# Performance work log

Hardware: AMD Instinct MI355X
Metric: run time of the kernel (lower is better)

The kernel has to match this reference:

```python
import jax, jax.numpy as jnp
import numpy as np

B, C, N = 16, 128, 2048  # batch, channels (SA_Layer(128)), num points


def setup_inputs() -> dict:
    key = jax.random.key(0)
    ks = jax.random.split(key, 6)
    x = jax.random.normal(ks[0], (B, C, N), jnp.float32)
    wq = jax.random.normal(ks[1], (C // 4, C), jnp.float32) * 0.05  # shared q/k 1x1 conv, no bias
    wv = jax.random.normal(ks[2], (C, C), jnp.float32) * 0.05
    bv = jax.random.normal(ks[3], (C,), jnp.float32) * 0.05
    wt = jax.random.normal(ks[4], (C, C), jnp.float32) * 0.05
    bt = jax.random.normal(ks[5], (C,), jnp.float32) * 0.05
    gamma = jnp.ones((C,), jnp.float32)   # BatchNorm1d weight
    beta = jnp.zeros((C,), jnp.float32)   # BatchNorm1d bias
    bn_mean = jnp.zeros((C,), jnp.float32)  # running mean (eval mode)
    bn_var = jnp.ones((C,), jnp.float32)    # running var (eval mode)
    return dict(x=x, wq=wq, wv=wv, bv=bv, wt=wt, bt=bt,
                gamma=gamma, beta=beta, bn_mean=bn_mean, bn_var=bn_var)


def reference(x, wq, wv, bv, wt, bt, gamma, beta, bn_mean, bn_var):
    EPS = 1e-9
    BN_EPS = 1e-5
    # q_conv and k_conv share weights (tied in __init__)
    x_q = jnp.einsum('dc,bcn->bnd', wq, x)               # [B, N, C/4]
    x_k = jnp.einsum('dc,bcn->bdn', wq, x)               # [B, C/4, N]
    energy = jnp.einsum('bnd,bdm->bnm', x_q, x_k)        # [B, N, N]
    attn = jax.nn.softmax(energy, axis=-1)
    # offset-attention renormalization: divide by column sum
    attn = attn / (EPS + attn.sum(axis=1, keepdims=True))
    x_v = jnp.einsum('dc,bcn->bdn', wv, x) + bv[None, :, None]   # [B, C, N]
    x_r = jnp.einsum('bdn,bnm->bdm', x_v, attn)                  # [B, C, N]
    t = jnp.einsum('dc,bcn->bdn', wt, x - x_r) + bt[None, :, None]
    # BatchNorm1d (eval mode) + ReLU
    t = (t - bn_mean[None, :, None]) * jax.lax.rsqrt(bn_var + BN_EPS)[None, :, None]
    t = t * gamma[None, :, None] + beta[None, :, None]
    return x + jax.nn.relu(t)
```

## Files before the change

### kernel.cpp

```cpp
#include <hip/hip_runtime.h>
#include <hip/hip_bf16.h>
#include <math.h>

#define BB 16
#define CC 128
#define NN 2048
#define CQ 32

typedef __attribute__((ext_vector_type(8))) short bf16x8;
typedef __attribute__((ext_vector_type(4))) float f32x4;
typedef __attribute__((ext_vector_type(16))) float f32x16;

__device__ __forceinline__ ushort f2b(float f) {
    __hip_bfloat16 h = __float2bfloat16(f);
    return *reinterpret_cast<ushort*>(&h);
}
__device__ __forceinline__ float b2f(ushort u) {
    union { unsigned u; float f; } v; v.u = ((unsigned)u) << 16;
    return v.f;
}
__device__ __forceinline__ bf16x8 as_b8(uint4 u) {
    union { uint4 u; bf16x8 b; } v; v.u = u; return v.b;
}
__device__ __forceinline__ float fexp2(float x) {
    return __builtin_amdgcn_exp2f(x);
}

#define OFF_VB  524288
#define OFF_XRB 2621440
#define OFF_RSI 4718592

#define QSCALE 1.2011224087864498f

__global__ __launch_bounds__(256) void k_proj(const float* __restrict__ x,
        const float* __restrict__ wq, const float* __restrict__ wv,
        const float* __restrict__ bv, ushort* __restrict__ Qt, ushort* __restrict__ Vb) {
    __shared__ ushort Wl[160][136];
    __shared__ ushort Xs[64][136];
    int bid = (blockIdx.x & 7) * 64 + (blockIdx.x >> 3);
    int b  = bid >> 5;
    int n0 = (bid & 31) << 6;
    int tid = threadIdx.x;
    #pragma unroll
    for (int k = 0; k < 20; ++k) {
        int idx = k * 256 + tid;
        int r = idx >> 5, c4 = (idx & 31) << 2;
        const float* srcw = (r < 32) ? (wq + r * 128 + c4) : (wv + (r - 32) * 128 + c4);
        float4 w4 = *(const float4*)srcw;
        float s = (r < 32) ? QSCALE : 1.0f;
        *(ushort4*)&Wl[r][c4] = make_ushort4(f2b(w4.x * s), f2b(w4.y * s),
                                             f2b(w4.z * s), f2b(w4.w * s));
    }
    const float* xb = x + (size_t)b * CC * NN;
    for (int idx = tid; idx < 2048; idx += 256) {
        int c = idx >> 4, n4 = (idx & 15) << 2;
        float4 xv = *(const float4*)&xb[c * NN + n0 + n4];
        Xs[n4][c]     = f2b(xv.x);
        Xs[n4 + 1][c] = f2b(xv.y);
        Xs[n4 + 2][c] = f2b(xv.z);
        Xs[n4 + 3][c] = f2b(xv.w);
    }
    __syncthreads();
    int w = tid >> 6, l = tid & 63, lr = l & 15, lg = l >> 4;
    f32x4 zero = {0.f, 0.f, 0.f, 0.f};
    int nn = n0 + w * 16 + lr;
    for (int dt = 0; dt < 10; ++dt) {
        f32x4 acc = zero;
        #pragma unroll
        for (int k = 0; k < 4; ++k) {
            bf16x8 a  = *(const bf16x8*)&Wl[dt * 16 + lr][k * 32 + lg * 8];
            bf16x8 bx = *(const bf16x8*)&Xs[w * 16 + lr][k * 32 + lg * 8];
            acc = __builtin_amdgcn_mfma_f32_16x16x32_bf16(a, bx, acc, 0, 0, 0);
        }
        if (dt < 2) {
            ushort4 p = make_ushort4(f2b(acc[0]), f2b(acc[1]), f2b(acc[2]), f2b(acc[3]));
            *(ushort4*)&Qt[(size_t)(b * NN + nn) * CQ + dt * 16 + lg * 4] = p;
        } else {
            #pragma unroll
            for (int i = 0; i < 4; ++i) {
                int vd = (dt - 2) * 16 + lg * 4 + i;
                Vb[(size_t)(b * CC + vd) * NN + nn] = f2b(acc[i] + bv[vd]);
            }
        }
    }
}

__global__ __launch_bounds__(512) void k_rowstats(const ushort* __restrict__ Qt,
        float* __restrict__ RSI) {
    __shared__ ushort Qm[128][36];
    __shared__ float Sred[2][64];
    int bid = (blockIdx.x & 7) * 64 + (blockIdx.x >> 3);
    int b  = bid >> 5;
    int n0 = (bid & 31) << 6;
    int tid = threadIdx.x;
    int w = tid >> 6, l = tid & 63, lr = l & 15, lg = l >> 4;
    int wn = w & 3, wm = w >> 2;
    const ushort* Qtb = Qt + (size_t)b * NN * CQ;
    bf16x8 aq = *(const bf16x8*)&Qtb[(size_t)(n0 + wn * 16 + lr) * CQ + lg * 8];
    int sr = tid >> 2, sc = (tid & 3) * 8;
    uint4 q0 = *(const uint4*)&Qtb[(size_t)sr * CQ + sc];
    float S[4] = {0.f, 0.f, 0.f, 0.f};
    f32x4 zero = {0.f, 0.f, 0.f, 0.f};
    for (int t = 0; t < 16; ++t) {
        __syncthreads();
        *(uint4*)&Qm[sr][sc] = q0;
        __syncthreads();
        if (t < 15)
            q0 = *(const uint4*)&Qtb[(size_t)((t + 1) * 128 + sr) * CQ + sc];
        #pragma unroll
        for (int mi = 0; mi < 4; ++mi) {
            bf16x8 bq = *(const bf16x8*)&Qm[(wm * 4 + mi) * 16 + lr][lg * 8];
            f32x4 e = __builtin_amdgcn_mfma_f32_16x16x32_bf16(aq, bq, zero, 0, 0, 0);
            S[0] += fexp2(e[0]); S[1] += fexp2(e[1]);
            S[2] += fexp2(e[2]); S[3] += fexp2(e[3]);
        }
    }
    #pragma unroll
    for (int d = 1; d < 16; d <<= 1) {
        #pragma unroll
        for (int i = 0; i < 4; ++i) S[i] += __shfl_xor(S[i], d);
    }
    if (lr == 0) {
        #pragma unroll
        for (int i = 0; i < 4; ++i) Sred[wm][wn * 16 + lg * 4 + i] = S[i];
    }
    __syncthreads();
    if (tid < 64)
        RSI[b * NN + n0 + tid] = 1.f / (Sred[0][tid] + Sred[1][tid]);
}

__global__ __launch_bounds__(512, 4) void k_attn_pv(const ushort* __restrict__ Qt,
        const ushort* __restrict__ Vb, const float* __restrict__ RSI,
        ushort* __restrict__ XRb) {
    __shared__ ushort Vs[2][128][68];
    __shared__ ushort Ws[2][64][68];
    __shared__ float csred[4][64];
    __shared__ float csum[64];
    int bid = (blockIdx.x & 7) * 64 + (blockIdx.x >> 3);
    int b  = bid >> 5;
    int m0 = (bid & 31) << 6;
    int tid = threadIdx.x;
    int w = tid >> 6, l = tid & 63, lr = l & 15, lg = l >> 4;
    const ushort* Qtb = Qt + (size_t)b * NN * CQ;
    const ushort* Vbb = Vb + (size_t)b * CC * NN;
    const float*  RSb = RSI + (size_t)b * NN;
    f32x4 zero = {0.f, 0.f, 0.f, 0.f};
    bool producer = (w < 4);

    bf16x8 bm[4];
    float cs[4] = {0.f, 0.f, 0.f, 0.f};
    int sv = 0, shv = 0;
    const ushort* vsrc = nullptr;
    bf16x8 aq_nx; float4 rsi_nx;
    f32x16 pacc0, pacc1;
    int ar = l & 31, kh = l >> 5, dq = w - 4;

    if (producer) {
        #pragma unroll
        for (int mi = 0; mi < 4; ++mi)
            bm[mi] = *(const bf16x8*)&Qtb[(size_t)(m0 + mi * 16 + lr) * CQ + lg * 8];
        sv = tid >> 1; shv = (tid & 1) * 32;
        vsrc = Vbb + (size_t)sv * NN + shv;
        {
            uint4 v0 = *(const uint4*)(vsrc);
            uint4 v1 = *(const uint4*)(vsrc + 8);
            uint4 v2 = *(const uint4*)(vsrc + 16);
            uint4 v3 = *(const uint4*)(vsrc + 24);
            ushort* dst = &Vs[0][sv][shv];
            *(uint2*)(dst)      = make_uint2(v0.x, v0.y);
            *(uint2*)(dst + 4)  = make_uint2(v0.z, v0.w);
            *(uint2*)(dst + 8)  = make_uint2(v1.x, v1.y);
            *(uint2*)(dst + 12) = make_uint2(v1.z, v1.w);
            *(uint2*)(dst + 16) = make_uint2(v2.x, v2.y);
            *(uint2*)(dst + 20) = make_uint2(v2.z, v2.w);
            *(uint2*)(dst + 24) = make_uint2(v3.x, v3.y);
            *(uint2*)(dst + 28) = make_uint2(v3.z, v3.w);
        }
        {
            bf16x8 aq0 = *(const bf16x8*)&Qtb[(size_t)(w * 16 + lr) * CQ + lg * 8];
            float4 r4 = *(const float4*)&RSb[w * 16 + lg * 4];
            int nb = w * 16 + lg * 4;
            #pragma unroll
            for (int mi = 0; mi < 4; ++mi) {
                f32x4 e = __builtin_amdgcn_mfma_f32_16x16x32_bf16(aq0, bm[mi], zero, 0, 0, 0);
                float w0 = fexp2(e[0]) * r4.x;
                float w1 = fexp2(e[1]) * r4.y;
                float w2 = fexp2(e[2]) * r4.z;
                float w3 = fexp2(e[3]) * r4.w;
                cs[mi] += w0 + w1 + w2 + w3;
                *(ushort4*)&Ws[0][mi * 16 + lr][nb] =
                    make_ushort4(f2b(w0), f2b(w1), f2b(w2), f2b(w3));
            }
        }
        aq_nx  = *(const bf16x8*)&Qtb[(size_t)(64 + w * 16 + lr) * CQ + lg * 8];
        rsi_nx = *(const float4*)&RSb[64 + w * 16 + lg * 4];
    } else {
        #pragma unroll
        for (int r = 0; r < 16; ++r) { pacc0[r] = 0.f; pacc1[r] = 0.f; }
    }
    __syncthreads();
    for (int t = 0; t < 32; ++t) {
        int cur = t & 1;
        if (producer) {
            if (t < 31) {
                int ntn = (t + 1) * 64;
                uint4 v0 = *(const uint4*)(vsrc + ntn);
                uint4 v1 = *(const uint4*)(vsrc + ntn + 8);
                uint4 v2 = *(const uint4*)(vsrc + ntn + 16);
                uint4 v3 = *(const uint4*)(vsrc + ntn + 24);
                bf16x8 aq = aq_nx;
                float4 r4 = rsi_nx;
                if (t < 30) {
                    int nt2 = (t + 2) * 64;
                    aq_nx  = *(const bf16x8*)&Qtb[(size_t)(nt2 + w * 16 + lr) * CQ + lg * 8];
                    rsi_nx = *(const float4*)&RSb[nt2 + w * 16 + lg * 4];
                }
                int nb = w * 16 + lg * 4;
                #pragma unroll
                for (int mi = 0; mi < 4; ++mi) {
                    f32x4 e = __builtin_amdgcn_mfma_f32_16x16x32_bf16(aq, bm[mi], zero, 0, 0, 0);
                    float w0 = fexp2(e[0]) * r4.x;
                    float w1 = fexp2(e[1]) * r4.y;
                    float w2 = fexp2(e[2]) * r4.z;
                    float w3 = fexp2(e[3]) * r4.w;
                    cs[mi] += w0 + w1 + w2 + w3;
                    *(ushort4*)&Ws[cur ^ 1][mi * 16 + lr][nb] =
                        make_ushort4(f2b(w0), f2b(w1), f2b(w2), f2b(w3));
                }
                ushort* dst = &Vs[cur ^ 1][sv][shv];
                *(uint2*)(dst)      = make_uint2(v0.x, v0.y);
                *(uint2*)(dst + 4)  = make_uint2(v0.z, v0.w);
                *(uint2*)(dst + 8)  = make_uint2(v1.x, v1.y);
                *(uint2*)(dst + 12) = make_uint2(v1.z, v1.w);
                *(uint2*)(dst + 16) = make_uint2(v2.x, v2.y);
                *(uint2*)(dst + 20) = make_uint2(v2.z, v2.w);
                *(uint2*)(dst + 24) = make_uint2(v3.x, v3.y);
                *(uint2*)(dst + 28) = make_uint2(v3.z, v3.w);
            }
        } else {
            __builtin_amdgcn_s_setprio(1);
            #pragma unroll
            for (int kk = 0; kk < 4; ++kk) {
                const ushort* vp = &Vs[cur][dq * 32 + ar][kk * 16 + kh * 8];
                uint2 a0 = *(const uint2*)vp;
                uint2 a1 = *(const uint2*)(vp + 4);
                bf16x8 va = as_b8(make_uint4(a0.x, a0.y, a1.x, a1.y));
                const ushort* wp0 = &Ws[cur][ar][kk * 16 + kh * 8];
                uint2 b0 = *(const uint2*)wp0;
                uint2 b1 = *(const uint2*)(wp0 + 4);
                const ushort* wp1 = &Ws[cur][32 + ar][kk * 16 + kh * 8];
                uint2 c0 = *(const uint2*)wp1;
                uint2 c1 = *(const uint2*)(wp1 + 4);
                pacc0 = __builtin_amdgcn_mfma_f32_32x32x16_bf16(
                    va, as_b8(make_uint4(b0.x, b0.y, b1.x, b1.y)), pacc0, 0, 0, 0);
                pacc1 = __builtin_amdgcn_mfma_f32_32x32x16_bf16(
                    va, as_b8(make_uint4(c0.x, c0.y, c1.x, c1.y)), pacc1, 0, 0, 0);
            }
            __builtin_amdgcn_s_setprio(0);
        }
        __syncthreads();
    }
    if (producer) {
        #pragma unroll
        for (int mi = 0; mi < 4; ++mi) {
            cs[mi] += __shfl_xor(cs[mi], 16);
            cs[mi] += __shfl_xor(cs[mi], 32);
        }
        if (lg == 0) {
            #pragma unroll
            for (int mi = 0; mi < 4; ++mi) csred[w][mi * 16 + lr] = cs[mi];
        }
    }
    __syncthreads();
    if (tid < 64) {
        float tot = csred[0][tid] + csred[1][tid] + csred[2][tid] + csred[3][tid];
        csum[tid] = 1.f / (1e-9f + tot);
    }
    __syncthreads();
    if (!producer) {
        float inv0 = csum[ar], inv1 = csum[32 + ar];
        #pragma unroll
        for (int r = 0; r < 16; ++r) {
            int d = dq * 32 + (r & 3) + 8 * (r >> 2) + 4 * kh;
            XRb[(size_t)(b * CC + d) * NN + m0 + ar]      = f2b(pacc0[r] * inv0);
            XRb[(size_t)(b * CC + d) * NN + m0 + 32 + ar] = f2b(pacc1[r] * inv1);
        }
    }
}

__global__ __launch_bounds__(256) void k_final(const float* __restrict__ x,
        const ushort* __restrict__ XRb, const float* __restrict__ wt,
        const float* __restrict__ bt, const float* __restrict__ gamma,
        const float* __restrict__ beta, const float* __restrict__ bn_mean,
        const float* __restrict__ bn_var, float* __restrict__ out) {
    __shared__ ushort Wl[128][136];
    __shared__ ushort Us[64][136];
    __shared__ float fAl[128], fBl[128];
    int bid = (blockIdx.x & 7) * 64 + (blockIdx.x >> 3);
    int b  = bid >> 5;
    int n0 = (bid & 31) << 6;
    int tid = threadIdx.x;
    #pragma unroll
    for (int k = 0; k < 16; ++k) {
        int idx = k * 256 + tid;
        int r = idx >> 5, c4 = (idx & 31) << 2;
        float4 w4 = *(const float4*)&wt[r * 128 + c4];
        *(ushort4*)&Wl[r][c4] = make_ushort4(f2b(w4.x), f2b(w4.y), f2b(w4.z), f2b(w4.w));
    }
    if (tid < 128) {
        float A = gamma[tid] * rsqrtf(bn_var[tid] + 1e-5f);
        fAl[tid] = A;
        fBl[tid] = (bt[tid] - bn_mean[tid]) * A + beta[tid];
    }
    const float*  xb  = x   + (size_t)b * CC * NN;
    const ushort* xrb = XRb + (size_t)b * CC * NN;
    for (int idx = tid; idx < 2048; idx += 256) {
        int c = idx >> 4, n4 = (idx & 15) << 2;
        float4 xv = *(const float4*)&xb[c * NN + n0 + n4];
        ushort4 rv = *(const ushort4*)&xrb[c * NN + n0 + n4];
        Us[n4][c]     = f2b(xv.x - b2f(rv.x));
        Us[n4 + 1][c] = f2b(xv.y - b2f(rv.y));
        Us[n4 + 2][c] = f2b(xv.z - b2f(rv.z));
        Us[n4 + 3][c] = f2b(xv.w - b2f(rv.w));
    }
    __syncthreads();
    int w = tid >> 6, l = tid & 63, lr = l & 15, lg = l >> 4;
    f32x4 zero = {0.f, 0.f, 0.f, 0.f};
    int nn = n0 + w * 16 + lr;
    for (int dt = 0; dt < 8; ++dt) {
        f32x4 acc = zero;
        #pragma unroll
        for (int k = 0; k < 4; ++k) {
            bf16x8 a  = *(const bf16x8*)&Wl[dt * 16 + lr][k * 32 + lg * 8];
            bf16x8 bx = *(const bf16x8*)&Us[w * 16 + lr][k * 32 + lg * 8];
            acc = __builtin_amdgcn_mfma_f32_16x16x32_bf16(a, bx, acc, 0, 0, 0);
        }
        #pragma unroll
        for (int i = 0; i < 4; ++i) {
            int r = dt * 16 + lg * 4 + i;
            float t = acc[i] * fAl[r] + fBl[r];
            t = fmaxf(t, 0.f);
            out[(size_t)(b * CC + r) * NN + nn] = xb[r * NN + nn] + t;
        }
    }
}

extern "C" void kernel_launch(void* const* d_in, const int* in_sizes, int n_in,
                              void* d_out, int out_size, void* d_ws, size_t ws_size,
                              hipStream_t stream) {
    const float* x       = (const float*)d_in[0];
    const float* wq      = (const float*)d_in[1];
    const float* wv      = (const float*)d_in[2];
    const float* bv      = (const float*)d_in[3];
    const float* wt      = (const float*)d_in[4];
    const float* bt      = (const float*)d_in[5];
    const float* gamma   = (const float*)d_in[6];
    const float* beta    = (const float*)d_in[7];
    const float* bn_mean = (const float*)d_in[8];
    const float* bn_var  = (const float*)d_in[9];
    float* out = (float*)d_out;
    float* ws  = (float*)d_ws;

    ushort* Qt   = (ushort*)ws;
    ushort* Vbp  = (ushort*)(ws + OFF_VB);
    ushort* XRb  = (ushort*)(ws + OFF_XRB);
    float*  RSI  = ws + OFF_RSI;

    k_proj<<<BB * 32, 256, 0, stream>>>(x, wq, wv, bv, Qt, Vbp);
    k_rowstats<<<BB * 32, 512, 0, stream>>>(Qt, RSI);
    k_attn_pv<<<BB * 32, 512, 0, stream>>>(Qt, Vbp, RSI, XRb);
    k_final<<<BB * 32, 256, 0, stream>>>(x, XRb, wt, bt, gamma, beta, bn_mean, bn_var, out);
}
```

Baseline: 70.44 us.

## Widen attention-PV tile to 128 output columns with 8 producer and 4 consumer warps

The fused attention-times-V kernel now gives each block 128 output columns instead of 64. Eight producer waves compute the bf16 attention weights and four consumer waves each hold a 64x64 accumulator tile built from four 32x32 MFMA accumulators. The goal is to halve how often V is re-read from global memory and to raise MFMA work per LDS load. In exchange the grid is halved to 256 blocks of 768 threads, which cuts parallelism and occupancy and raises LDS and register pressure.

```diff
diff --git a/kernel.cpp b/kernel.cpp
--- a/kernel.cpp
+++ b/kernel.cpp
@@ -129,57 +129,54 @@
         RSI[b * NN + n0 + tid] = 1.f / (Sred[0][tid] + Sred[1][tid]);
 }
 
-__global__ __launch_bounds__(512, 4) void k_attn_pv(const ushort* __restrict__ Qt,
+__global__ __launch_bounds__(768, 3) void k_attn_pv(const ushort* __restrict__ Qt,
         const ushort* __restrict__ Vb, const float* __restrict__ RSI,
         ushort* __restrict__ XRb) {
     __shared__ ushort Vs[2][128][68];
-    __shared__ ushort Ws[2][64][68];
-    __shared__ float csred[4][64];
-    __shared__ float csum[64];
-    int bid = (blockIdx.x & 7) * 64 + (blockIdx.x >> 3);
-    int b  = bid >> 5;
-    int m0 = (bid & 31) << 6;
+    __shared__ ushort Ws[2][128][68];
+    __shared__ float csred[4][128];
+    __shared__ float csum[128];
+    int bid = (blockIdx.x & 7) * 32 + (blockIdx.x >> 3);
+    int b  = bid >> 4;
+    int m0 = (bid & 15) << 7;
     int tid = threadIdx.x;
     int w = tid >> 6, l = tid & 63, lr = l & 15, lg = l >> 4;
     const ushort* Qtb = Qt + (size_t)b * NN * CQ;
     const ushort* Vbb = Vb + (size_t)b * CC * NN;
     const float*  RSb = RSI + (size_t)b * NN;
     f32x4 zero = {0.f, 0.f, 0.f, 0.f};
-    bool producer = (w < 4);
-
+    bool producer = (w < 8);
+
+    int wn = w & 3, mh = w >> 2;
     bf16x8 bm[4];
     float cs[4] = {0.f, 0.f, 0.f, 0.f};
     int sv = 0, shv = 0;
     const ushort* vsrc = nullptr;
     bf16x8 aq_nx; float4 rsi_nx;
-    f32x16 pacc0, pacc1;
-    int ar = l & 31, kh = l >> 5, dq = w - 4;
+    int cw = w - 8;
+    int dh = cw >> 1, mh2 = cw & 1;
+    int ar = l & 31, kh = l >> 5;
+    f32x16 pacc00, pacc01, pacc10, pacc11;
 
     if (producer) {
         #pragma unroll
         for (int mi = 0; mi < 4; ++mi)
-            bm[mi] = *(const bf16x8*)&Qtb[(size_t)(m0 + mi * 16 + lr) * CQ + lg * 8];
-        sv = tid >> 1; shv = (tid & 1) * 32;
+            bm[mi] = *(const bf16x8*)&Qtb[(size_t)(m0 + (mh * 4 + mi) * 16 + lr) * CQ + lg * 8];
+        sv = tid >> 2; shv = (tid & 3) * 16;
         vsrc = Vbb + (size_t)sv * NN + shv;
         {
             uint4 v0 = *(const uint4*)(vsrc);
             uint4 v1 = *(const uint4*)(vsrc + 8);
-            uint4 v2 = *(const uint4*)(vsrc + 16);
-            uint4 v3 = *(const uint4*)(vsrc + 24);
             ushort* dst = &Vs[0][sv][shv];
             *(uint2*)(dst)      = make_uint2(v0.x, v0.y);
             *(uint2*)(dst + 4)  = make_uint2(v0.z, v0.w);
             *(uint2*)(dst + 8)  = make_uint2(v1.x, v1.y);
             *(uint2*)(dst + 12) = make_uint2(v1.z, v1.w);
-            *(uint2*)(dst + 16) = make_uint2(v2.x, v2.y);
-            *(uint2*)(dst + 20) = make_uint2(v2.z, v2.w);
-            *(uint2*)(dst + 24) = make_uint2(v3.x, v3.y);
-            *(uint2*)(dst + 28) = make_uint2(v3.z, v3.w);
         }
         {
-            bf16x8 aq0 = *(const bf16x8*)&Qtb[(size_t)(w * 16 + lr) * CQ + lg * 8];
-            float4 r4 = *(const float4*)&RSb[w * 16 + lg * 4];
-            int nb = w * 16 + lg * 4;
+            bf16x8 aq0 = *(const bf16x8*)&Qtb[(size_t)(wn * 16 + lr) * CQ + lg * 8];
+            float4 r4 = *(const float4*)&RSb[wn * 16 + lg * 4];
+            int nb = wn * 16 + lg * 4;
             #pragma unroll
             for (int mi = 0; mi < 4; ++mi) {
                 f32x4 e = __builtin_amdgcn_mfma_f32_16x16x32_bf16(aq0, bm[mi], zero, 0, 0, 0);
@@ -188,15 +185,17 @@
                 float w2 = fexp2(e[2]) * r4.z;
                 float w3 = fexp2(e[3]) * r4.w;
                 cs[mi] += w0 + w1 + w2 + w3;
-                *(ushort4*)&Ws[0][mi * 16 + lr][nb] =
+                *(ushort4*)&Ws[0][(mh * 4 + mi) * 16 + lr][nb] =
                     make_ushort4(f2b(w0), f2b(w1), f2b(w2), f2b(w3));
             }
         }
-        aq_nx  = *(const bf16x8*)&Qtb[(size_t)(64 + w * 16 + lr) * CQ + lg * 8];
-        rsi_nx = *(const float4*)&RSb[64 + w * 16 + lg * 4];
+        aq_nx  = *(const bf16x8*)&Qtb[(size_t)(64 + wn * 16 + lr) * CQ + lg * 8];
+        rsi_nx = *(const float4*)&RSb[64 + wn * 16 + lg * 4];
     } else {
         #pragma unroll
-        for (int r = 0; r < 16; ++r) { pacc0[r] = 0.f; pacc1[r] = 0.f; }
+        for (int r = 0; r < 16; ++r) {
+            pacc00[r] = 0.f; pacc01[r] = 0.f; pacc10[r] = 0.f; pacc11[r] = 0.f;
+        }
     }
     __syncthreads();
     for (int t = 0; t < 32; ++t) {
@@ -206,16 +205,14 @@
                 int ntn = (t + 1) * 64;
                 uint4 v0 = *(const uint4*)(vsrc + ntn);
                 uint4 v1 = *(const uint4*)(vsrc + ntn + 8);
-                uint4 v2 = *(const uint4*)(vsrc + ntn + 16);
-                uint4 v3 = *(const uint4*)(vsrc + ntn + 24);
                 bf16x8 aq = aq_nx;
                 float4 r4 = rsi_nx;
                 if (t < 30) {
                     int nt2 = (t + 2) * 64;
-                    aq_nx  = *(const bf16x8*)&Qtb[(size_t)(nt2 + w * 16 + lr) * CQ + lg * 8];
-                    rsi_nx = *(const float4*)&RSb[nt2 + w * 16 + lg * 4];
+                    aq_nx  = *(const bf16x8*)&Qtb[(size_t)(nt2 + wn * 16 + lr) * CQ + lg * 8];
+                    rsi_nx = *(const float4*)&RSb[nt2 + wn * 16 + lg * 4];
                 }
-                int nb = w * 16 + lg * 4;
+                int nb = wn * 16 + lg * 4;
                 #pragma unroll
                 for (int mi = 0; mi < 4; ++mi) {
                     f32x4 e = __builtin_amdgcn_mfma_f32_16x16x32_bf16(aq, bm[mi], zero, 0, 0, 0);
@@ -224,7 +221,7 @@
                     float w2 = fexp2(e[2]) * r4.z;
                     float w3 = fexp2(e[3]) * r4.w;
                     cs[mi] += w0 + w1 + w2 + w3;
-                    *(ushort4*)&Ws[cur ^ 1][mi * 16 + lr][nb] =
+                    *(ushort4*)&Ws[cur ^ 1][(mh * 4 + mi) * 16 + lr][nb] =
                         make_ushort4(f2b(w0), f2b(w1), f2b(w2), f2b(w3));
                 }
                 ushort* dst = &Vs[cur ^ 1][sv][shv];
@@ -232,29 +229,27 @@
                 *(uint2*)(dst + 4)  = make_uint2(v0.z, v0.w);
                 *(uint2*)(dst + 8)  = make_uint2(v1.x, v1.y);
                 *(uint2*)(dst + 12) = make_uint2(v1.z, v1.w);
-                *(uint2*)(dst + 16) = make_uint2(v2.x, v2.y);
-                *(uint2*)(dst + 20) = make_uint2(v2.z, v2.w);
-                *(uint2*)(dst + 24) = make_uint2(v3.x, v3.y);
-                *(uint2*)(dst + 28) = make_uint2(v3.z, v3.w);
             }
         } else {
             __builtin_amdgcn_s_setprio(1);
             #pragma unroll
             for (int kk = 0; kk < 4; ++kk) {
-                const ushort* vp = &Vs[cur][dq * 32 + ar][kk * 16 + kh * 8];
-                uint2 a0 = *(const uint2*)vp;
-                uint2 a1 = *(const uint2*)(vp + 4);
-                bf16x8 va = as_b8(make_uint4(a0.x, a0.y, a1.x, a1.y));
-                const ushort* wp0 = &Ws[cur][ar][kk * 16 + kh * 8];
-                uint2 b0 = *(const uint2*)wp0;
-                uint2 b1 = *(const uint2*)(wp0 + 4);
-                const ushort* wp1 = &Ws[cur][32 + ar][kk * 16 + kh * 8];
-                uint2 c0 = *(const uint2*)wp1;
-                uint2 c1 = *(const uint2*)(wp1 + 4);
-                pacc0 = __builtin_amdgcn_mfma_f32_32x32x16_bf16(
-                    va, as_b8(make_uint4(b0.x, b0.y, b1.x, b1.y)), pacc0, 0, 0, 0);
-                pacc1 = __builtin_amdgcn_mfma_f32_32x32x16_bf16(
-                    va, as_b8(make_uint4(c0.x, c0.y, c1.x, c1.y)), pacc1, 0, 0, 0);
+                const ushort* vp0 = &Vs[cur][dh * 64 + ar][kk * 16 + kh * 8];
+                const ushort* vp1 = &Vs[cur][dh * 64 + 32 + ar][kk * 16 + kh * 8];
+                uint2 a0 = *(const uint2*)vp0; uint2 a1 = *(const uint2*)(vp0 + 4);
+                uint2 a2 = *(const uint2*)vp1; uint2 a3 = *(const uint2*)(vp1 + 4);
+                bf16x8 va0 = as_b8(make_uint4(a0.x, a0.y, a1.x, a1.y));
+                bf16x8 va1 = as_b8(make_uint4(a2.x, a2.y, a3.x, a3.y));
+                const ushort* wp0 = &Ws[cur][mh2 * 64 + ar][kk * 16 + kh * 8];
+                const ushort* wp1 = &Ws[cur][mh2 * 64 + 32 + ar][kk * 16 + kh * 8];
+                uint2 b0 = *(const uint2*)wp0; uint2 b1 = *(const uint2*)(wp0 + 4);
+                uint2 c0 = *(const uint2*)wp1; uint2 c1 = *(const uint2*)(wp1 + 4);
+                bf16x8 wb0 = as_b8(make_uint4(b0.x, b0.y, b1.x, b1.y));
+                bf16x8 wb1 = as_b8(make_uint4(c0.x, c0.y, c1.x, c1.y));
+                pacc00 = __builtin_amdgcn_mfma_f32_32x32x16_bf16(va0, wb0, pacc00, 0, 0, 0);
+                pacc01 = __builtin_amdgcn_mfma_f32_32x32x16_bf16(va0, wb1, pacc01, 0, 0, 0);
+                pacc10 = __builtin_amdgcn_mfma_f32_32x32x16_bf16(va1, wb0, pacc10, 0, 0, 0);
+                pacc11 = __builtin_amdgcn_mfma_f32_32x32x16_bf16(va1, wb1, pacc11, 0, 0, 0);
             }
             __builtin_amdgcn_s_setprio(0);
         }
@@ -268,22 +263,27 @@
         }
         if (lg == 0) {
             #pragma unroll
-            for (int mi = 0; mi < 4; ++mi) csred[w][mi * 16 + lr] = cs[mi];
-        }
-    }
-    __syncthreads();
-    if (tid < 64) {
+            for (int mi = 0; mi < 4; ++mi)
+                csred[wn][(mh * 4 + mi) * 16 + lr] = cs[mi];
+        }
+    }
+    __syncthreads();
+    if (tid < 128) {
         float tot = csred[0][tid] + csred[1][tid] + csred[2][tid] + csred[3][tid];
         csum[tid] = 1.f / (1e-9f + tot);
     }
     __syncthreads();
     if (!producer) {
-        float inv0 = csum[ar], inv1 = csum[32 + ar];
+        float inv0 = csum[mh2 * 64 + ar];
+        float inv1 = csum[mh2 * 64 + 32 + ar];
+        int mA = m0 + mh2 * 64 + ar;
         #pragma unroll
         for (int r = 0; r < 16; ++r) {
-            int d = dq * 32 + (r & 3) + 8 * (r >> 2) + 4 * kh;
-            XRb[(size_t)(b * CC + d) * NN + m0 + ar]      = f2b(pacc0[r] * inv0);
-            XRb[(size_t)(b * CC + d) * NN + m0 + 32 + ar] = f2b(pacc1[r] * inv1);
+            int d0 = dh * 64 + (r & 3) + 8 * (r >> 2) + 4 * kh;
+            XRb[(size_t)(b * CC + d0) * NN + mA]          = f2b(pacc00[r] * inv0);
+            XRb[(size_t)(b * CC + d0) * NN + mA + 32]     = f2b(pacc01[r] * inv1);
+            XRb[(size_t)(b * CC + d0 + 32) * NN + mA]      = f2b(pacc10[r] * inv0);
+            XRb[(size_t)(b * CC + d0 + 32) * NN + mA + 32] = f2b(pacc11[r] * inv1);
         }
     }
 }
@@ -368,6 +368,6 @@
 
     k_proj<<<BB * 32, 256, 0, stream>>>(x, wq, wv, bv, Qt, Vbp);
     k_rowstats<<<BB * 32, 512, 0, stream>>>(Qt, RSI);
-    k_attn_pv<<<BB * 32, 512, 0, stream>>>(Qt, Vbp, RSI, XRb);
+    k_attn_pv<<<BB * 16, 768, 0, stream>>>(Qt, Vbp, RSI, XRb);
     k_final<<<BB * 32, 256, 0, stream>>>(x, XRb, wt, bt, gamma, beta, bn_mean, bn_var, out);
 }
```

Result: faster. 66.98 us (-4.9%).
